# Performance work log

Measured on AMD Instinct MI355X. Metric: run time of the kernel, lower is better.

Reference implementation:

```python
import jax, jax.numpy as jnp
import numpy as np

B, C, H, W = 8, 128, 128, 128

def setup_inputs() -> dict:
    key = jax.random.key(0)
    ks = jax.random.split(key, 6)
    s = 1.0 / np.sqrt(C)
    return {
        "x": jax.random.normal(ks[0], (B, C, H, W), dtype=jnp.float32),
        "w_qkv": jax.random.uniform(ks[1], (3 * C, C), jnp.float32, -s, s),
        "w_gate": jax.random.uniform(ks[2], (C, C), jnp.float32, -s, s),
        "b_gate": jax.random.uniform(ks[3], (C,), jnp.float32, -s, s),
        "w_proj": jax.random.uniform(ks[4], (C, C), jnp.float32, -s, s),
        "b_proj": jax.random.uniform(ks[5], (C,), jnp.float32, -s, s),
    }

def reference(x, w_qkv, w_gate, b_gate, w_proj, b_proj):
    b, c, h, w = x.shape
    n = h * w
    # [b,c,h,w] -> [b,n,c]
    x_seq = jnp.transpose(x, (0, 2, 3, 1)).reshape(b, n, c)
    # SiLU gate on spatial-domain features
    t = jax.nn.silu(x_seq @ w_gate.T + b_gate)  # [b,n,c]
    x_sp = x_seq.reshape(b, h, w, c)
    # frequency domain (ortho norm carries the 1/N factor)
    x_fft = jnp.fft.rfft2(x_sp, axes=(1, 2), norm="ortho")  # [b,h,w//2+1,c] complex64
    # complex linear with real weight == apply weight to real & imag parts
    qkv = jnp.einsum("bhwc,dc->bhwd", x_fft, w_qkv.astype(x_fft.dtype))
    q, k, v = jnp.split(qkv, 3, axis=-1)
    # eq.15: a = F^{-1}(conj(F(Q)) * F(K))
    attn = jnp.fft.irfft2(jnp.conj(q) * k, s=(h, w), axes=(1, 2), norm="ortho")
    # softmax over the flattened spatial axis n
    attn = jax.nn.softmax(attn.reshape(b, n, c), axis=1).reshape(b, h, w, c)
    # eq.16: O = F^{-1}(conj(F(sigma(a))) * F(V)); note forward rfft2 uses default (backward) norm
    attn_f = jnp.fft.rfft2(attn, axes=(1, 2))
    out = jnp.fft.irfft2(jnp.conj(attn_f) * v, s=(h, w), axes=(1, 2), norm="ortho")
    out = out.reshape(b, n, c) * t
    out = out @ w_proj.T + b_proj
    return jnp.transpose(out.reshape(b, h, w, c), (0, 3, 1, 2))
```

## Files before the change

### kernel.cpp

```cpp
#include <hip/hip_runtime.h>
#include <math.h>


constexpr int CH    = 128;
constexpr int NSP   = 128 * 128;
constexpr int BATCH = 8;
constexpr int NIMG  = BATCH * CH;
constexpr int RS    = 130;
constexpr int NT    = 1024;
constexpr int NW    = NT / 64;


typedef short short8 __attribute__((ext_vector_type(8)));
typedef float f32x4  __attribute__((ext_vector_type(4)));
union U8 { unsigned u[4]; short8 s; };

__device__ __forceinline__ unsigned bf16r(float x) {
  unsigned u = __float_as_uint(x);
  return (u + 0x7FFFu + ((u >> 16) & 1u)) >> 16;
}
__device__ __forceinline__ float bflo(unsigned w) { return __uint_as_float(w << 16); }
__device__ __forceinline__ float bfhi(unsigned w) { return __uint_as_float(w & 0xFFFF0000u); }

__device__ __forceinline__ void split_pair(float e0, float e1,
                                           unsigned& hi, unsigned& lo) {
  const unsigned u0 = __float_as_uint(e0), u1 = __float_as_uint(e1);
  hi = (u0 >> 16) | (u1 & 0xFFFF0000u);
  const float r0 = e0 - __uint_as_float(u0 & 0xFFFF0000u);
  const float r1 = e1 - __uint_as_float(u1 & 0xFFFF0000u);
  lo = bf16r(r0) | (bf16r(r1) << 16);
}

__device__ __forceinline__ void load_a_frag(const float* wr, short8& ah, short8& al) {
  const float4 wa = *(const float4*)wr;
  const float4 wb = *(const float4*)(wr + 4);
  U8 hi, lo;
  split_pair(wa.x, wa.y, hi.u[0], lo.u[0]);
  split_pair(wa.z, wa.w, hi.u[1], lo.u[1]);
  split_pair(wb.x, wb.y, hi.u[2], lo.u[2]);
  split_pair(wb.z, wb.w, hi.u[3], lo.u[3]);
  ah = hi.s; al = lo.s;
}


__global__ void prep_weights(const float* __restrict__ w_qkv,
                             const float* __restrict__ w_gate,
                             const float* __restrict__ w_proj,
                             short* __restrict__ wpre) {
  const int t = blockIdx.x * 256 + threadIdx.x;
  const int lane = t & 63;
  const int mf   = (t >> 6) & 3;
  const int kg   = (t >> 8) & 3;
  const int mbi  = (t >> 10) & 1;
  const int g    = t >> 11;
  if (g >= 5) return;
  const float* W = (g < 3) ? (w_qkv + (size_t)g * CH * CH)
                           : (g == 3 ? w_gate : w_proj);
  const int row = mbi * 64 + mf * 16 + (lane & 15);
  const int k0  = kg * 32 + (lane >> 4) * 8;
  short8 ah, al;
  load_a_frag(W + (size_t)row * CH + k0, ah, al);
  const size_t base = ((size_t)(g * 2 + mbi) * 16 + kg * 4 + mf) * 1024;
  *(short8*)(wpre + base + lane * 8)       = ah;
  *(short8*)(wpre + base + 512 + lane * 8) = al;
}


__device__ __forceinline__ void mfma_half(const short8* __restrict__ wf,
                                          const short8 bh[4], const short8 bl[4],
                                          f32x4 acc[4][4], int kg, int lane) {
  short8 ah[4], al[4];
#pragma unroll
  for (int mf = 0; mf < 4; ++mf) {
    const short8* p = wf + (kg * 4 + mf) * 128 + lane;
    ah[mf] = p[0];
    al[mf] = p[64];
  }
#pragma unroll
  for (int mf = 0; mf < 4; ++mf)
#pragma unroll
    for (int nf = 0; nf < 4; ++nf)
      acc[mf][nf] = __builtin_amdgcn_mfma_f32_16x16x32_bf16(al[mf], bh[nf], acc[mf][nf], 0, 0, 0);
#pragma unroll
  for (int mf = 0; mf < 4; ++mf)
#pragma unroll
    for (int nf = 0; nf < 4; ++nf)
      acc[mf][nf] = __builtin_amdgcn_mfma_f32_16x16x32_bf16(ah[mf], bl[nf], acc[mf][nf], 0, 0, 0);
#pragma unroll
  for (int mf = 0; mf < 4; ++mf)
#pragma unroll
    for (int nf = 0; nf < 4; ++nf)
      acc[mf][nf] = __builtin_amdgcn_mfma_f32_16x16x32_bf16(ah[mf], bh[nf], acc[mf][nf], 0, 0, 0);
}

__device__ __forceinline__ void mfma_core2(const unsigned* xs,
                                           const short8* __restrict__ wfA,
                                           const short8* __restrict__ wfB,
                                           f32x4 aA[4][4], f32x4 aB[4][4], int tid) {
  const int lane = tid & 63, wid = tid >> 6;
  const int nb = (wid & 1) * 64;
  const int lm = lane & 15, quad = lane >> 4;
#pragma unroll
  for (int kg = 0; kg < 4; ++kg) {
    short8 bh[4], bl[4];
    const int kwb = (kg * 16 + quad * 4) ^ (lm << 2);
#pragma unroll
    for (int nf = 0; nf < 4; ++nf) {
      const unsigned* p = xs + (nb + nf * 16 + lm) * 64 + kwb;
      bh[nf] = *(const short8*)p;
      bl[nf] = *(const short8*)(p + 8192);
    }
    mfma_half(wfA, bh, bl, aA, kg, lane);
    mfma_half(wfB, bh, bl, aB, kg, lane);
  }
}

__device__ __forceinline__ void mfma_core1(const unsigned* xs,
                                           const short8* __restrict__ wf,
                                           f32x4 acc[4][4], int tid) {
  const int lane = tid & 63, wid = tid >> 6;
  const int nb = (wid & 1) * 64;
  const int lm = lane & 15, quad = lane >> 4;
#pragma unroll
  for (int kg = 0; kg < 4; ++kg) {
    short8 bh[4], bl[4];
    const int kwb = (kg * 16 + quad * 4) ^ (lm << 2);
#pragma unroll
    for (int nf = 0; nf < 4; ++nf) {
      const unsigned* p = xs + (nb + nf * 16 + lm) * 64 + kwb;
      bh[nf] = *(const short8*)p;
      bl[nf] = *(const short8*)(p + 8192);
    }
    mfma_half(wf, bh, bl, acc, kg, lane);
  }
}


__global__ __launch_bounds__(256, 2)
void gemm_qkvg(const float* __restrict__ x, const short* __restrict__ wpre,
               const float* __restrict__ b_gate,
               unsigned* __restrict__ QKp, unsigned short* __restrict__ Vp,
               float* __restrict__ Tp) {
  __shared__ __align__(16) unsigned xs[16384];
  __shared__ __align__(16) float bounce[4 * 528];
  const int tid = threadIdx.x;
  const int n0 = blockIdx.x * 128;
  const int b  = blockIdx.y;
  const float* xb = x + (size_t)b * CH * NSP;

  {
    const int tn = tid >> 3;
    const int tk = tid & 7;
#pragma unroll
    for (int i = 0; i < 8; ++i) {
      const int k = 2 * tk + 16 * i;
      const float* p0 = xb + (size_t)k * NSP + n0 + 4 * tn;
      const float4 a = *(const float4*)p0;
      const float4 c = *(const float4*)(p0 + NSP);
      const float a4[4] = {a.x, a.y, a.z, a.w};
      const float c4[4] = {c.x, c.y, c.z, c.w};
      const int kw = tk + 8 * i;
#pragma unroll
      for (int j = 0; j < 4; ++j) {
        const int nn = 4 * tn + j;
        unsigned hi, lo;
        split_pair(a4[j], c4[j], hi, lo);
        const int kws = kw ^ ((nn & 15) << 2);
        xs[nn * 64 + kws] = hi;
        xs[8192 + nn * 64 + kws] = lo;
      }
    }
  }
  __syncthreads();

  const int lane = tid & 63, wid = tid >> 6;
  const int mb = (wid >> 1) * 64, nb = (wid & 1) * 64;
  const int lm = lane & 15, quad = lane >> 4;
  const int mbi = wid >> 1;
  const short8* wp = (const short8*)wpre;
  const short8* wQ = wp + (size_t)(0 * 2 + mbi) * 2048;
  const short8* wK = wp + (size_t)(1 * 2 + mbi) * 2048;
  const short8* wV = wp + (size_t)(2 * 2 + mbi) * 2048;
  const short8* wG = wp + (size_t)(3 * 2 + mbi) * 2048;
  float* const bw = bounce + wid * 528;
  unsigned* const ubw = (unsigned*)bw;

  f32x4 aq[4][4], ak[4][4];
#pragma unroll
  for (int mf = 0; mf < 4; ++mf)
#pragma unroll
    for (int nf = 0; nf < 4; ++nf) { aq[mf][nf] = (f32x4){0,0,0,0}; ak[mf][nf] = (f32x4){0,0,0,0}; }
  mfma_core2(xs, wQ, wK, aq, ak, tid);

#pragma unroll
  for (int mf = 0; mf < 4; ++mf) {
#pragma unroll
    for (int half = 0; half < 2; ++half) {
#pragma unroll
      for (int nn = 0; nn < 2; ++nn) {
        const int nf = half * 2 + nn;
#pragma unroll
        for (int i = 0; i < 4; ++i)
          ubw[(quad * 4 + i) * 33 + nn * 16 + lm] =
              bf16r(aq[mf][nf][i]) | (bf16r(ak[mf][nf][i]) << 16);
      }
#pragma unroll
      for (int j = 0; j < 2; ++j) {
        const int rl = (lane >> 3) + 8 * j;
        const int cl = (lane & 7) * 4;
        const uint4 v = *(const uint4*)(ubw + rl * 33 + cl);
        const int row = mb + mf * 16 + rl;
        *(uint4*)(QKp + ((size_t)b * CH + row) * NSP + n0 + nb + half * 32 + cl) = v;
      }
    }
  }

  f32x4 av[4][4], at[4][4];
#pragma unroll
  for (int mf = 0; mf < 4; ++mf)
#pragma unroll
    for (int nf = 0; nf < 4; ++nf) { av[mf][nf] = (f32x4){0,0,0,0}; at[mf][nf] = (f32x4){0,0,0,0}; }
  mfma_core2(xs, wV, wG, av, at, tid);

#pragma unroll
  for (int mf = 0; mf < 4; ++mf) {
#pragma unroll
    for (int half = 0; half < 2; ++half) {
#pragma unroll
      for (int nn = 0; nn < 2; ++nn) {
        const int nf = half * 2 + nn;
#pragma unroll
        for (int i = 0; i < 4; ++i)
          bw[(quad * 4 + i) * 33 + nn * 16 + lm] = av[mf][nf][i];
      }
#pragma unroll
      for (int j = 0; j < 2; ++j) {
        const int rl = (lane >> 3) + 8 * j;
        const int cl = (lane & 7) * 4;
        const float4 v = *(const float4*)(bw + rl * 33 + cl);
        const int row = mb + mf * 16 + rl;
        uint2 pv;
        pv.x = bf16r(v.x) | (bf16r(v.y) << 16);
        pv.y = bf16r(v.z) | (bf16r(v.w) << 16);
        *(uint2*)(Vp + ((size_t)b * CH + row) * NSP + n0 + nb + half * 32 + cl) = pv;
      }
    }
  }

#pragma unroll
  for (int mf = 0; mf < 4; ++mf) {
#pragma unroll
    for (int half = 0; half < 2; ++half) {
#pragma unroll
      for (int nn = 0; nn < 2; ++nn) {
        const int nf = half * 2 + nn;
#pragma unroll
        for (int i = 0; i < 4; ++i)
          bw[(quad * 4 + i) * 33 + nn * 16 + lm] = at[mf][nf][i];
      }
#pragma unroll
      for (int j = 0; j < 2; ++j) {
        const int rl = (lane >> 3) + 8 * j;
        const int cl = (lane & 7) * 4;
        float4 v = *(const float4*)(bw + rl * 33 + cl);
        const int row = mb + mf * 16 + rl;
        const float bg = b_gate[row];
        float e[4] = {v.x, v.y, v.z, v.w};
#pragma unroll
        for (int q = 0; q < 4; ++q) {
          const float g = e[q] + bg;
          e[q] = g / (1.0f + __expf(-g));
        }
        v = make_float4(e[0], e[1], e[2], e[3]);
        *(float4*)(Tp + ((size_t)b * CH + row) * NSP + n0 + nb + half * 32 + cl) = v;
      }
    }
  }
}


__device__ __forceinline__ void acc_to_bounce(float* bounce, f32x4 acc[4][4], int tid) {
  const int lane = tid & 63, wid = tid >> 6;
  const int mb = (wid >> 1) * 64;
  const int nb = (wid & 1) * 64;
  const int lm = lane & 15, quad = lane >> 4;
#pragma unroll
  for (int mf = 0; mf < 4; ++mf)
#pragma unroll
    for (int nf = 0; nf < 4; ++nf) {
      const int col = nb + nf * 16 + lm;
      const int r0 = mb + mf * 16 + quad * 4;
#pragma unroll
      for (int i = 0; i < 4; ++i)
        bounce[(r0 + i) * 132 + col] = acc[mf][nf][i];
    }
}

__global__ __launch_bounds__(256, 2)
void gemm_proj(const unsigned short* __restrict__ OC, const float* __restrict__ Tn,
               const short* __restrict__ wpre, const float* __restrict__ b_proj,
               float* __restrict__ outp) {
  __shared__ __align__(16) unsigned xs[16896];
  const int tid = threadIdx.x;
  const int n0 = blockIdx.x * 128;
  const int b = blockIdx.y;
  const unsigned short* ob = OC + (size_t)b * CH * NSP;
  const float* tb = Tn + (size_t)b * CH * NSP;

  {
    const int tn = tid >> 3;
    const int tk = tid & 7;
#pragma unroll
    for (int i = 0; i < 8; ++i) {
      const int k = 2 * tk + 16 * i;
      const uint2 ou0 = *(const uint2*)(ob + (size_t)k * NSP + n0 + 4 * tn);
      const uint2 ou1 = *(const uint2*)(ob + (size_t)(k + 1) * NSP + n0 + 4 * tn);
      const float* pt = tb + (size_t)k * NSP + n0 + 4 * tn;
      const float4 t0 = *(const float4*)pt;
      const float4 t1 = *(const float4*)(pt + NSP);
      const float z0[4] = {bflo(ou0.x) * t0.x, bfhi(ou0.x) * t0.y,
                           bflo(ou0.y) * t0.z, bfhi(ou0.y) * t0.w};
      const float z1[4] = {bflo(ou1.x) * t1.x, bfhi(ou1.x) * t1.y,
                           bflo(ou1.y) * t1.z, bfhi(ou1.y) * t1.w};
      const int kw = tk + 8 * i;
#pragma unroll
      for (int j = 0; j < 4; ++j) {
        const int nn = 4 * tn + j;
        unsigned hi, lo;
        split_pair(z0[j], z1[j], hi, lo);
        const int kws = kw ^ ((nn & 15) << 2);
        xs[nn * 64 + kws] = hi;
        xs[8192 + nn * 64 + kws] = lo;
      }
    }
  }
  __syncthreads();

  const int mbi = (tid >> 6) >> 1;
  const short8* wP = (const short8*)wpre + (size_t)(4 * 2 + mbi) * 2048;

  f32x4 acc[4][4];
#pragma unroll
  for (int mf = 0; mf < 4; ++mf)
#pragma unroll
    for (int nf = 0; nf < 4; ++nf) acc[mf][nf] = (f32x4){0,0,0,0};

  mfma_core1(xs, wP, acc, tid);

  __syncthreads();
  float* bounce = (float*)xs;
  acc_to_bounce(bounce, acc, tid);
  __syncthreads();

  const int rr = tid >> 5;
  const int c4i = (tid & 31) * 4;
#pragma unroll
  for (int i = 0; i < 16; ++i) {
    const int row = rr + 8 * i;
    const float bp = b_proj[row];
    float4 v = *(const float4*)(bounce + row * 132 + c4i);
    v.x += bp; v.y += bp; v.z += bp; v.w += bp;
    *(float4*)(outp + ((size_t)b * CH + row) * NSP + n0 + c4i) = v;
  }
}


__device__ __forceinline__ float2 cmul(float2 a, float2 b) {
  return make_float2(fmaf(a.x, b.x, -(a.y * b.y)), fmaf(a.x, b.y, a.y * b.x));
}
#define CADD(a,b) make_float2((a).x+(b).x,(a).y+(b).y)
#define CSUB(a,b) make_float2((a).x-(b).x,(a).y-(b).y)
#define MULNI(t)  make_float2((t).y, -(t).x)
constexpr float C45 = 0.7071067811865476f;

__device__ __forceinline__ void fft8(float2* x) {
  float2 t;
  t = CSUB(x[0],x[4]); x[0]=CADD(x[0],x[4]); x[4]=t;
  t = CSUB(x[1],x[5]); x[1]=CADD(x[1],x[5]); x[5]=make_float2(C45*(t.x+t.y), C45*(t.y-t.x));
  t = CSUB(x[2],x[6]); x[2]=CADD(x[2],x[6]); x[6]=MULNI(t);
  t = CSUB(x[3],x[7]); x[3]=CADD(x[3],x[7]); x[7]=make_float2(C45*(t.y-t.x), -C45*(t.x+t.y));
  t = CSUB(x[0],x[2]); x[0]=CADD(x[0],x[2]); x[2]=t;
  t = CSUB(x[1],x[3]); x[1]=CADD(x[1],x[3]); x[3]=MULNI(t);
  t = CSUB(x[4],x[6]); x[4]=CADD(x[4],x[6]); x[6]=t;
  t = CSUB(x[5],x[7]); x[5]=CADD(x[5],x[7]); x[7]=MULNI(t);
  t = CSUB(x[0],x[1]); x[0]=CADD(x[0],x[1]); x[1]=t;
  t = CSUB(x[2],x[3]); x[2]=CADD(x[2],x[3]); x[3]=t;
  t = CSUB(x[4],x[5]); x[4]=CADD(x[4],x[5]); x[5]=t;
  t = CSUB(x[6],x[7]); x[6]=CADD(x[6],x[7]); x[7]=t;
}

__device__ __forceinline__ void fft16(float2* z) {
  float2 t;
  t=CSUB(z[0],z[8]);   z[0]=CADD(z[0],z[8]);   z[8]=t;
  t=CSUB(z[1],z[9]);   z[1]=CADD(z[1],z[9]);   z[9]=cmul(t,  make_float2( 0.9238795325f,-0.3826834324f));
  t=CSUB(z[2],z[10]);  z[2]=CADD(z[2],z[10]);  z[10]=make_float2(C45*(t.x+t.y), C45*(t.y-t.x));
  t=CSUB(z[3],z[11]);  z[3]=CADD(z[3],z[11]);  z[11]=cmul(t, make_float2( 0.3826834324f,-0.9238795325f));
  t=CSUB(z[4],z[12]);  z[4]=CADD(z[4],z[12]);  z[12]=MULNI(t);
  t=CSUB(z[5],z[13]);  z[5]=CADD(z[5],z[13]);  z[13]=cmul(t, make_float2(-0.3826834324f,-0.9238795325f));
  t=CSUB(z[6],z[14]);  z[6]=CADD(z[6],z[14]);  z[14]=make_float2(C45*(t.y-t.x), -C45*(t.x+t.y));
  t=CSUB(z[7],z[15]);  z[7]=CADD(z[7],z[15]);  z[15]=cmul(t, make_float2(-0.9238795325f,-0.3826834324f));
  t=CSUB(z[0],z[4]);   z[0]=CADD(z[0],z[4]);   z[4]=t;
  t=CSUB(z[1],z[5]);   z[1]=CADD(z[1],z[5]);   z[5]=make_float2(C45*(t.x+t.y), C45*(t.y-t.x));
  t=CSUB(z[2],z[6]);   z[2]=CADD(z[2],z[6]);   z[6]=MULNI(t);
  t=CSUB(z[3],z[7]);   z[3]=CADD(z[3],z[7]);   z[7]=make_float2(C45*(t.y-t.x), -C45*(t.x+t.y));
  t=CSUB(z[8],z[12]);  z[8]=CADD(z[8],z[12]);  z[12]=t;
  t=CSUB(z[9],z[13]);  z[9]=CADD(z[9],z[13]);  z[13]=make_float2(C45*(t.x+t.y), C45*(t.y-t.x));
  t=CSUB(z[10],z[14]); z[10]=CADD(z[10],z[14]); z[14]=MULNI(t);
  t=CSUB(z[11],z[15]); z[11]=CADD(z[11],z[15]); z[15]=make_float2(C45*(t.y-t.x), -C45*(t.x+t.y));
  t=CSUB(z[0],z[2]);   z[0]=CADD(z[0],z[2]);   z[2]=t;
  t=CSUB(z[1],z[3]);   z[1]=CADD(z[1],z[3]);   z[3]=MULNI(t);
  t=CSUB(z[4],z[6]);   z[4]=CADD(z[4],z[6]);   z[6]=t;
  t=CSUB(z[5],z[7]);   z[5]=CADD(z[5],z[7]);   z[7]=MULNI(t);
  t=CSUB(z[8],z[10]);  z[8]=CADD(z[8],z[10]);  z[10]=t;
  t=CSUB(z[9],z[11]);  z[9]=CADD(z[9],z[11]);  z[11]=MULNI(t);
  t=CSUB(z[12],z[14]); z[12]=CADD(z[12],z[14]); z[14]=t;
  t=CSUB(z[13],z[15]); z[13]=CADD(z[13],z[15]); z[15]=MULNI(t);
  t=CSUB(z[0],z[1]);   z[0]=CADD(z[0],z[1]);   z[1]=t;
  t=CSUB(z[2],z[3]);   z[2]=CADD(z[2],z[3]);   z[3]=t;
  t=CSUB(z[4],z[5]);   z[4]=CADD(z[4],z[5]);   z[5]=t;
  t=CSUB(z[6],z[7]);   z[6]=CADD(z[6],z[7]);   z[7]=t;
  t=CSUB(z[8],z[9]);   z[8]=CADD(z[8],z[9]);   z[9]=t;
  t=CSUB(z[10],z[11]); z[10]=CADD(z[10],z[11]); z[11]=t;
  t=CSUB(z[12],z[13]); z[12]=CADD(z[12],z[13]); z[13]=t;
  t=CSUB(z[14],z[15]); z[14]=CADD(z[14],z[15]); z[15]=t;
}

template<int SPT, int SLN, int SRC, int EPI>
__device__ __forceinline__ void fft_pass(float2* img, const float2* tw,
                                         int lane, int wid,
                                         const unsigned* gqk,
                                         const unsigned short* gv,
                                         float escale, float& lsum) {
  const int n2 = lane & 15, rr = lane >> 4;
  constexpr int br3[8] = {0,4,2,6,1,5,3,7};
#pragma unroll
  for (int u = 0; u < 2; ++u) {
    const int line = wid * 8 + u * 4 + rr;
    const int lb = SLN * line;
    float2 x[8];
    if constexpr (SRC == 0) {
#pragma unroll
      for (int n1 = 0; n1 < 8; ++n1) x[n1] = img[lb + SPT * (16 * n1 + n2)];
    } else if constexpr (SRC == 1) {
#pragma unroll
      for (int n1 = 0; n1 < 8; ++n1) {
        const unsigned qk = gqk[line * 128 + 16 * n1 + n2];
        x[n1] = make_float2(bflo(qk), bfhi(qk));
      }
    } else {
#pragma unroll
      for (int n1 = 0; n1 < 8; ++n1) {
        const float a = img[lb + SPT * (16 * n1 + n2)].x;
        const unsigned short vv = gv[line * 128 + 16 * n1 + n2];
        x[n1] = make_float2(a, __uint_as_float((unsigned)vv << 16));
      }
    }
    fft8(x);
#pragma unroll
    for (int m = 0; m < 8; ++m) {
      const int k1 = br3[m];
      const float2 y = (k1 == 0) ? x[m] : cmul(x[m], tw[k1 - 1]);
      img[lb + SPT * (16 * k1 + (n2 ^ k1))] = y;
    }
  }
  const int k1 = lane & 7;
  const int lb = SLN * (wid * 8 + (lane >> 3));
  const int kb = 16 * k1;
  float2 z[16];
#pragma unroll
  for (int j = 0; j < 16; ++j) z[j] = img[lb + SPT * (kb + (j ^ k1))];
  fft16(z);
  constexpr int br4[16] = {0,8,4,12,2,10,6,14,1,9,5,13,3,11,7,15};
#pragma unroll
  for (int m = 0; m < 16; ++m) {
    const int a = lb + SPT * (k1 + 8 * br4[m]);
    if constexpr (EPI == 1) {
      const float ex = __expf(z[m].x * escale);
      lsum += ex;
      img[a] = make_float2(ex, 0.0f);
    } else {
      img[a] = z[m];
    }
  }
}

__device__ __forceinline__ void cross_spectrum(float2* img, int tid) {
#pragma unroll
  for (int i = 0; i < 8; ++i) {
    const int pid = tid + (i << 10);
    int fr, fc;
    if (pid < 8064)      { fc = 1 + (pid >> 7); fr = pid & 127; }
    else if (pid < 8127) { fc = 0;  fr = pid - 8063; }
    else if (pid < 8190) { fc = 64; fr = pid - 8126; }
    else if (pid == 8190) {
#pragma unroll
      for (int s = 0; s < 4; ++s) {
        const int a = ((s >> 1) * 64) * RS + (s & 1) * 64;
        const float2 zz = img[a];
        img[a] = make_float2(zz.x * zz.y, 0.0f);
      }
      continue;
    } else continue;
    const int gr = (128 - fr) & 127, gc = 128 - fc >= 128 ? 0 : (128 - fc) & 127;
    const int f = fr * RS + fc, g = gr * RS + gc;
    const float2 zf = img[f], zg = img[g];
    const float qr = 0.5f * (zf.x + zg.x), qi = 0.5f * (zf.y - zg.y);
    const float kr = 0.5f * (zf.y + zg.y), ki = 0.5f * (zg.x - zf.x);
    const float yr = qr * kr + qi * ki;
    const float yi = qr * ki - qi * kr;
    img[f] = make_float2(yr, -yi);
    img[g] = make_float2(yr, yi);
  }
}

__global__ __launch_bounds__(NT)
void fft_attn_fused(const unsigned* __restrict__ QKin,
                    const unsigned short* __restrict__ Vin,
                    unsigned short* __restrict__ Out) {
  __shared__ float2 img[128 * RS];
  __shared__ float red[NW];
  const int tid = threadIdx.x, lane = tid & 63, wid = tid >> 6;
  const size_t off = (size_t)blockIdx.x * NSP;
  const unsigned* gqk = QKin + off;
  const unsigned short* gv = Vin + off;

  float2 tw[7];
  {
    const int n2 = lane & 15;
#pragma unroll
    for (int k = 1; k < 8; ++k) {
      float s, c;
      sincosf(6.283185307179586f * (float)(n2 * k) * (1.0f / 128.0f), &s, &c);
      tw[k - 1] = make_float2(c, -s);
    }
  }
  float dummy = 0.0f;

  fft_pass<1, RS, 1, 0>(img, tw, lane, wid, gqk, nullptr, 0.0f, dummy);
  __syncthreads();
  fft_pass<RS, 1, 0, 0>(img, tw, lane, wid, nullptr, nullptr, 0.0f, dummy);
  __syncthreads();
  cross_spectrum(img, tid);
  __syncthreads();
  const float escale = 1.0f / 2097152.0f;
  float lsum = 0.0f;
  fft_pass<1, RS, 0, 0>(img, tw, lane, wid, nullptr, nullptr, 0.0f, dummy);
  __syncthreads();
  fft_pass<RS, 1, 0, 1>(img, tw, lane, wid, nullptr, nullptr, escale, lsum);
  __syncthreads();

#pragma unroll
  for (int s = 32; s >= 1; s >>= 1) lsum += __shfl_xor(lsum, s, 64);
  if (lane == 0) red[wid] = lsum;
  __syncthreads();
  float tot = 0.0f;
#pragma unroll
  for (int w = 0; w < NW; ++w) tot += red[w];
  const float inv = 1.0f / tot;

  fft_pass<1, RS, 2, 0>(img, tw, lane, wid, nullptr, gv, 0.0f, dummy);
  __syncthreads();
  fft_pass<RS, 1, 0, 0>(img, tw, lane, wid, nullptr, nullptr, 0.0f, dummy);
  __syncthreads();
  cross_spectrum(img, tid);
  __syncthreads();
  fft_pass<1, RS, 0, 0>(img, tw, lane, wid, nullptr, nullptr, 0.0f, dummy);
  __syncthreads();
  fft_pass<RS, 1, 0, 0>(img, tw, lane, wid, nullptr, nullptr, 0.0f, dummy);
  __syncthreads();

  const float os = inv * (1.0f / 16384.0f);
#pragma unroll
  for (int i = 0; i < 4; ++i) {
    const int e = (tid + i * NT) * 4;
    const float2* base = img + (e >> 7) * RS + (e & 127);
    const float4 a = *(const float4*)base;
    const float4 c = *(const float4*)(base + 2);
    uint2 o;
    o.x = bf16r(a.x * os) | (bf16r(a.z * os) << 16);
    o.y = bf16r(c.x * os) | (bf16r(c.z * os) << 16);
    *(uint2*)(Out + off + e) = o;
  }
}


extern "C" void kernel_launch(void* const* d_in, const int* in_sizes, int n_in,
                              void* d_out, int out_size, void* d_ws, size_t ws_size,
                              hipStream_t stream) {
  const float* x      = (const float*)d_in[0];
  const float* w_qkv  = (const float*)d_in[1];
  const float* w_gate = (const float*)d_in[2];
  const float* b_gate = (const float*)d_in[3];
  const float* w_proj = (const float*)d_in[4];
  const float* b_proj = (const float*)d_in[5];
  float* outp = (float*)d_out;

  const size_t SZ = (size_t)BATCH * CH * NSP;
  char* base = (char*)d_ws;
  unsigned*       QK = (unsigned*)base;
  unsigned short* V  = (unsigned short*)(base + SZ * 4);
  float*          T  = (float*)(base + SZ * 6);
  unsigned short* OC = (unsigned short*)(base + SZ * 10);
  short*          WP = (short*)(base + SZ * 12);

  prep_weights<<<40, 256, 0, stream>>>(w_qkv, w_gate, w_proj, WP);

  dim3 g1(128, BATCH);
  gemm_qkvg<<<g1, 256, 0, stream>>>(x, WP, b_gate, QK, V, T);

  fft_attn_fused<<<NIMG, NT, 0, stream>>>(QK, V, OC);

  dim3 g2(128, BATCH);
  gemm_proj<<<g2, 256, 0, stream>>>(OC, T, WP, b_proj, outp);
}
```

Measured before the change: 346.0 us.

## Vectorize shared-memory FFT passes with paired-line float4 accesses and new swizzle

```diff
diff --git a/kernel.cpp b/kernel.cpp
--- a/kernel.cpp
+++ b/kernel.cpp
@@ -425,55 +425,101 @@
   t=CSUB(z[14],z[15]); z[14]=CADD(z[14],z[15]); z[15]=t;
 }
 
-template<int SPT, int SLN, int SRC, int EPI>
-__device__ __forceinline__ void fft_pass(float2* img, const float2* tw,
-                                         int lane, int wid,
-                                         const unsigned* gqk,
-                                         const unsigned short* gv,
-                                         float escale, float& lsum) {
-  const int n2 = lane & 15, rr = lane >> 4;
+template<int SRC>
+__device__ __forceinline__ void fft_row_pass(float2* img,
+                                             const float2* twA, const float2* twB,
+                                             int lane, int wid,
+                                             const unsigned* __restrict__ gqk,
+                                             const unsigned short* __restrict__ gv) {
+  const int c   = lane & 7;
+  const int row = wid * 8 + (lane >> 3);
+  const int lb  = RS * row;
   constexpr int br3[8] = {0,4,2,6,1,5,3,7};
-#pragma unroll
-  for (int u = 0; u < 2; ++u) {
-    const int line = wid * 8 + u * 4 + rr;
-    const int lb = SLN * line;
-    float2 x[8];
+  {
+    float2 xA[8], xB[8];
     if constexpr (SRC == 0) {
 #pragma unroll
-      for (int n1 = 0; n1 < 8; ++n1) x[n1] = img[lb + SPT * (16 * n1 + n2)];
+      for (int n1 = 0; n1 < 8; ++n1) {
+        const float4 v = *(const float4*)(img + lb + 16 * n1 + 2 * c);
+        xA[n1] = make_float2(v.x, v.y);
+        xB[n1] = make_float2(v.z, v.w);
+      }
     } else if constexpr (SRC == 1) {
 #pragma unroll
       for (int n1 = 0; n1 < 8; ++n1) {
-        const unsigned qk = gqk[line * 128 + 16 * n1 + n2];
-        x[n1] = make_float2(bflo(qk), bfhi(qk));
+        const uint2 qk = *(const uint2*)(gqk + row * 128 + 16 * n1 + 2 * c);
+        xA[n1] = make_float2(bflo(qk.x), bfhi(qk.x));
+        xB[n1] = make_float2(bflo(qk.y), bfhi(qk.y));
       }
     } else {
 #pragma unroll
       for (int n1 = 0; n1 < 8; ++n1) {
-        const float a = img[lb + SPT * (16 * n1 + n2)].x;
-        const unsigned short vv = gv[line * 128 + 16 * n1 + n2];
-        x[n1] = make_float2(a, __uint_as_float((unsigned)vv << 16));
-      }
-    }
-    fft8(x);
+        const float4 v = *(const float4*)(img + lb + 16 * n1 + 2 * c);
+        const unsigned vv = *(const unsigned*)(gv + row * 128 + 16 * n1 + 2 * c);
+        xA[n1] = make_float2(v.x, bflo(vv));
+        xB[n1] = make_float2(v.z, bfhi(vv));
+      }
+    }
+    fft8(xA); fft8(xB);
 #pragma unroll
     for (int m = 0; m < 8; ++m) {
       const int k1 = br3[m];
-      const float2 y = (k1 == 0) ? x[m] : cmul(x[m], tw[k1 - 1]);
-      img[lb + SPT * (16 * k1 + (n2 ^ k1))] = y;
-    }
-  }
-  const int k1 = lane & 7;
-  const int lb = SLN * (wid * 8 + (lane >> 3));
-  const int kb = 16 * k1;
+      const float2 yA = (k1 == 0) ? xA[m] : cmul(xA[m], twA[k1 - 1]);
+      const float2 yB = (k1 == 0) ? xB[m] : cmul(xB[m], twB[k1 - 1]);
+      const int d = c ^ (k1 >> 1);
+      *(float4*)(img + lb + 16 * k1 + 2 * d) = make_float4(yA.x, yA.y, yB.x, yB.y);
+    }
+  }
+  const int k1 = c;
   float2 z[16];
 #pragma unroll
-  for (int j = 0; j < 16; ++j) z[j] = img[lb + SPT * (kb + (j ^ k1))];
+  for (int t = 0; t < 8; ++t) {
+    const int u = t ^ (k1 >> 1);
+    const float4 v = *(const float4*)(img + lb + 16 * k1 + 2 * u);
+    z[2 * t]     = make_float2(v.x, v.y);
+    z[2 * t + 1] = make_float2(v.z, v.w);
+  }
   fft16(z);
   constexpr int br4[16] = {0,8,4,12,2,10,6,14,1,9,5,13,3,11,7,15};
 #pragma unroll
+  for (int m = 0; m < 16; ++m)
+    img[lb + k1 + 8 * br4[m]] = z[m];
+}
+
+template<int EPI>
+__device__ __forceinline__ void fft_col_pass(float2* img, const float2* twC,
+                                             int lane, int wid,
+                                             float escale, float& lsum) {
+  constexpr int br3[8] = {0,4,2,6,1,5,3,7};
+  {
+    const int n2 = lane & 15;
+    const int p  = wid * 4 + (lane >> 4);
+    float2 xA[8], xB[8];
+#pragma unroll
+    for (int n1 = 0; n1 < 8; ++n1) {
+      const float4 v = *(const float4*)(img + (16 * n1 + n2) * RS + 2 * p);
+      xA[n1] = make_float2(v.x, v.y);
+      xB[n1] = make_float2(v.z, v.w);
+    }
+    fft8(xA); fft8(xB);
+#pragma unroll
+    for (int m = 0; m < 8; ++m) {
+      const int k1 = br3[m];
+      const float2 yA = (k1 == 0) ? xA[m] : cmul(xA[m], twC[k1 - 1]);
+      const float2 yB = (k1 == 0) ? xB[m] : cmul(xB[m], twC[k1 - 1]);
+      *(float4*)(img + (16 * k1 + (n2 ^ k1)) * RS + 2 * p) = make_float4(yA.x, yA.y, yB.x, yB.y);
+    }
+  }
+  const int k1  = lane & 7;
+  const int col = wid * 8 + (lane >> 3);
+  float2 z[16];
+#pragma unroll
+  for (int j = 0; j < 16; ++j) z[j] = img[(16 * k1 + (j ^ k1)) * RS + col];
+  fft16(z);
+  constexpr int br4[16] = {0,8,4,12,2,10,6,14,1,9,5,13,3,11,7,15};
+#pragma unroll
   for (int m = 0; m < 16; ++m) {
-    const int a = lb + SPT * (k1 + 8 * br4[m]);
+    const int a = (k1 + 8 * br4[m]) * RS + col;
     if constexpr (EPI == 1) {
       const float ex = __expf(z[m].x * escale);
       lsum += ex;
@@ -488,20 +534,21 @@
 #pragma unroll
   for (int i = 0; i < 8; ++i) {
     const int pid = tid + (i << 10);
-    int fr, fc;
-    if (pid < 8064)      { fc = 1 + (pid >> 7); fr = pid & 127; }
-    else if (pid < 8127) { fc = 0;  fr = pid - 8063; }
-    else if (pid < 8190) { fc = 64; fr = pid - 8126; }
-    else if (pid == 8190) {
-#pragma unroll
-      for (int s = 0; s < 4; ++s) {
-        const int a = ((s >> 1) * 64) * RS + (s & 1) * 64;
-        const float2 zz = img[a];
-        img[a] = make_float2(zz.x * zz.y, 0.0f);
-      }
-      continue;
-    } else continue;
-    const int gr = (128 - fr) & 127, gc = 128 - fc >= 128 ? 0 : (128 - fc) & 127;
+    int fr = pid >> 6;
+    int fc = pid & 63;
+    if (fc == 0) {
+      if (fr >= 65) { fc = 64; fr -= 64; }
+      else if (fr == 0 || fr == 64) {
+        const int a0 = fr * RS;
+        const float2 z0 = img[a0];
+        img[a0] = make_float2(z0.x * z0.y, 0.0f);
+        const int a1 = fr * RS + 64;
+        const float2 z1 = img[a1];
+        img[a1] = make_float2(z1.x * z1.y, 0.0f);
+        continue;
+      }
+    }
+    const int gr = (128 - fr) & 127, gc = (128 - fc) & 127;
     const int f = fr * RS + fc, g = gr * RS + gc;
     const float2 zf = img[f], zg = img[g];
     const float qr = 0.5f * (zf.x + zg.x), qi = 0.5f * (zf.y - zg.y);
@@ -517,36 +564,42 @@
 void fft_attn_fused(const unsigned* __restrict__ QKin,
                     const unsigned short* __restrict__ Vin,
                     unsigned short* __restrict__ Out) {
-  __shared__ float2 img[128 * RS];
+  __shared__ __align__(16) float2 img[128 * RS];
   __shared__ float red[NW];
   const int tid = threadIdx.x, lane = tid & 63, wid = tid >> 6;
   const size_t off = (size_t)blockIdx.x * NSP;
   const unsigned* gqk = QKin + off;
   const unsigned short* gv = Vin + off;
 
-  float2 tw[7];
+  float2 twA[7], twB[7], twC[7];
   {
-    const int n2 = lane & 15;
+    const int c2  = (lane & 7) * 2;
+    const int n2c = lane & 15;
+    const float w = 6.283185307179586f * (1.0f / 128.0f);
 #pragma unroll
     for (int k = 1; k < 8; ++k) {
-      float s, c;
-      sincosf(6.283185307179586f * (float)(n2 * k) * (1.0f / 128.0f), &s, &c);
-      tw[k - 1] = make_float2(c, -s);
+      float s, cc;
+      sincosf(w * (float)(c2 * k), &s, &cc);
+      twA[k - 1] = make_float2(cc, -s);
+      sincosf(w * (float)((c2 + 1) * k), &s, &cc);
+      twB[k - 1] = make_float2(cc, -s);
+      sincosf(w * (float)(n2c * k), &s, &cc);
+      twC[k - 1] = make_float2(cc, -s);
     }
   }
   float dummy = 0.0f;
 
-  fft_pass<1, RS, 1, 0>(img, tw, lane, wid, gqk, nullptr, 0.0f, dummy);
-  __syncthreads();
-  fft_pass<RS, 1, 0, 0>(img, tw, lane, wid, nullptr, nullptr, 0.0f, dummy);
+  fft_row_pass<1>(img, twA, twB, lane, wid, gqk, nullptr);
+  __syncthreads();
+  fft_col_pass<0>(img, twC, lane, wid, 0.0f, dummy);
   __syncthreads();
   cross_spectrum(img, tid);
   __syncthreads();
   const float escale = 1.0f / 2097152.0f;
   float lsum = 0.0f;
-  fft_pass<1, RS, 0, 0>(img, tw, lane, wid, nullptr, nullptr, 0.0f, dummy);
-  __syncthreads();
-  fft_pass<RS, 1, 0, 1>(img, tw, lane, wid, nullptr, nullptr, escale, lsum);
+  fft_row_pass<0>(img, twA, twB, lane, wid, nullptr, nullptr);
+  __syncthreads();
+  fft_col_pass<1>(img, twC, lane, wid, escale, lsum);
   __syncthreads();
 
 #pragma unroll
@@ -558,15 +611,15 @@
   for (int w = 0; w < NW; ++w) tot += red[w];
   const float inv = 1.0f / tot;
 
-  fft_pass<1, RS, 2, 0>(img, tw, lane, wid, nullptr, gv, 0.0f, dummy);
-  __syncthreads();
-  fft_pass<RS, 1, 0, 0>(img, tw, lane, wid, nullptr, nullptr, 0.0f, dummy);
+  fft_row_pass<2>(img, twA, twB, lane, wid, nullptr, gv);
+  __syncthreads();
+  fft_col_pass<0>(img, twC, lane, wid, 0.0f, dummy);
   __syncthreads();
   cross_spectrum(img, tid);
   __syncthreads();
-  fft_pass<1, RS, 0, 0>(img, tw, lane, wid, nullptr, nullptr, 0.0f, dummy);
-  __syncthreads();
-  fft_pass<RS, 1, 0, 0>(img, tw, lane, wid, nullptr, nullptr, 0.0f, dummy);
+  fft_row_pass<0>(img, twA, twB, lane, wid, nullptr, nullptr);
+  __syncthreads();
+  fft_col_pass<0>(img, twC, lane, wid, 0.0f, dummy);
   __syncthreads();
 
   const float os = inv * (1.0f / 16384.0f);
```

Measured after the change: 451.2 us. 1.3x slower.
